# Performance work log

Measured on AMD Instinct MI355X. Metric: run time of the kernel, lower is better.

The kernel has to match this reference:

```python
import jax, jax.numpy as jnp
import numpy as np

B, C, L = 4, 64, 4096
RED = 4          # reduction -> q/k channels = C // RED = 16
N_HASHES = 4
HASH_BUCKETS = min(L // 4, 32)  # = 32, matches torch code
EPS = 1e-5


def _conv1x1(x, W, b):
    # x: [B, Cin, L], W: [Cout, Cin], b: [Cout]
    return jnp.einsum('bcl,oc->bol', x, W) + b[None, :, None]


def setup_inputs() -> dict:
    key = jax.random.key(0)
    ks = jax.random.split(key, 12)
    Cq = C // RED
    x = jax.random.normal(ks[0], (B, C, L), dtype=jnp.float32)
    hash_idx = jax.random.randint(ks[1], (B, N_HASHES, L), 0, HASH_BUCKETS, dtype=jnp.int32)
    sC = 1.0 / np.sqrt(C)
    Wq = jax.random.normal(ks[2], (Cq, C), dtype=jnp.float32) * sC
    bq = jax.random.normal(ks[3], (Cq,), dtype=jnp.float32) * 0.01
    Wk = jax.random.normal(ks[4], (Cq, C), dtype=jnp.float32) * sC
    bk = jax.random.normal(ks[5], (Cq,), dtype=jnp.float32) * 0.01
    Wv = jax.random.normal(ks[6], (C, C), dtype=jnp.float32) * sC
    bv = jax.random.normal(ks[7], (C,), dtype=jnp.float32) * 0.01
    Wo = jax.random.normal(ks[8], (C, C), dtype=jnp.float32) * sC
    bo = jax.random.normal(ks[9], (C,), dtype=jnp.float32) * 0.01
    gamma = jax.random.normal(ks[10], (1,), dtype=jnp.float32)  # nonzero so attn path matters
    bn_w = jnp.ones((C,), dtype=jnp.float32)
    bn_b = jnp.zeros((C,), dtype=jnp.float32)
    return dict(x=x, hash_idx=hash_idx, Wq=Wq, bq=bq, Wk=Wk, bk=bk,
                Wv=Wv, bv=bv, Wo=Wo, bo=bo, gamma=gamma, bn_w=bn_w, bn_b=bn_b)


def reference(x, hash_idx, Wq, bq, Wk, bk, Wv, bv, Wo, bo, gamma, bn_w, bn_b):
    # 1x1 conv projections
    q = _conv1x1(x, Wq, bq)   # [B, C/RED, L]
    k = _conv1x1(x, Wk, bk)   # [B, C/RED, L]
    v = _conv1x1(x, Wv, bv)   # [B, C, L]

    qT = q.transpose(0, 2, 1)  # [B, L, Cq]
    kT = k.transpose(0, 2, 1)
    vT = v.transpose(0, 2, 1)  # [B, L, C]

    # raw scores are hash-independent; only the bucket mask changes per hash
    scores = jnp.einsum('bic,bjc->bij', qT, kT)  # [B, L, L], no sqrt(d) scaling (matches torch)

    n_hashes = hash_idx.shape[1]
    acc = jnp.zeros_like(vT)
    for h in range(n_hashes):  # small fixed loop
        idx = hash_idx[:, h, :]                       # [B, L]
        mask = idx[:, :, None] == idx[:, None, :]     # same-bucket mask [B, L, L]
        s = jnp.where(mask, scores, -1e9)
        attn = jax.nn.softmax(s, axis=-1)             # within-bucket softmax (diag always valid)
        acc = acc + jnp.einsum('bij,bjc->bic', attn, vT)
    attn_out = (acc / n_hashes).transpose(0, 2, 1)    # [B, C, L], averaged over hashes

    out = _conv1x1(attn_out, Wo, bo)
    out = gamma * out + x                             # residual with learned scalar

    # BatchNorm1d, training mode: biased batch stats over (B, L) per channel
    mean = out.mean(axis=(0, 2), keepdims=True)
    var = out.var(axis=(0, 2), keepdims=True)
    out = (out - mean) * jax.lax.rsqrt(var + EPS)
    out = out * bn_w[None, :, None] + bn_b[None, :, None]
    return out
```

## Files before the change

kernel.cpp:

```cpp
#include <hip/hip_runtime.h>
#include <math.h>

#define Bn 4
#define Cn 64
#define Ln 4096
#define CQ 16
#define NH 4
#define NB 32
#define EPSV 1e-5f

#define MAXS 384
#define SFULL 192

#define QSZ   (Bn*Ln*CQ)
#define VSZ   (Bn*Ln*Cn)
#define ACCSZ (Bn*Ln*Cn)
#define NBH   (Bn*NH)

#define OFF_K   QSZ
#define OFF_V   (2*QSZ)
#define OFF_ACC (2*QSZ + VSZ)

#define LOG2E 1.44269504088896f

__global__ __launch_bounds__(256) void proj_kernel(
        const float* __restrict__ x,
        const float* __restrict__ Wq, const float* __restrict__ bq,
        const float* __restrict__ Wk, const float* __restrict__ bk,
        const float* __restrict__ Wv, const float* __restrict__ bv,
        float* __restrict__ q, float* __restrict__ k, float* __restrict__ v) {
    __shared__ float sWt[Cn*32];
    __shared__ float sb[32];
    int tid = threadIdx.x;
    int third = blockIdx.x % 3;
    int pg    = blockIdx.x / 3;
    int rbase = third * 32;
    for (int idx = tid; idx < Cn*32; idx += 256) {
        int rr = idx & 31, c = idx >> 5;
        int r = rbase + rr;
        float w;
        if (r < 16)      w = Wq[r*Cn + c];
        else if (r < 32) w = Wk[(r-16)*Cn + c];
        else             w = Wv[(r-32)*Cn + c];
        sWt[c*32 + rr] = w;
    }
    if (tid < 32) {
        int r = rbase + tid;
        sb[tid] = (r < 16) ? bq[r] : (r < 32 ? bk[r-16] : bv[r-32]);
    }
    __syncthreads();
    int p = tid & 63, og = tid >> 6;
    int gp = pg * 64 + p;
    int b = gp >> 12, l = gp & (Ln - 1);
    const float* xp = &x[b*Cn*Ln + l];
    int rr0 = og * 8;
    float val[8];
    #pragma unroll
    for (int i = 0; i < 8; i++) val[i] = sb[rr0 + i];
    #pragma unroll
    for (int c0 = 0; c0 < Cn; c0 += 8) {
        float xv[8];
        #pragma unroll
        for (int i = 0; i < 8; i++) xv[i] = xp[(c0 + i)*Ln];
        #pragma unroll
        for (int i = 0; i < 8; i++) {
            const float4 wa = *(const float4*)&sWt[(c0 + i)*32 + rr0];
            const float4 wb = *(const float4*)&sWt[(c0 + i)*32 + rr0 + 4];
            float xvi = xv[i];
            val[0] = fmaf(wa.x, xvi, val[0]); val[1] = fmaf(wa.y, xvi, val[1]);
            val[2] = fmaf(wa.z, xvi, val[2]); val[3] = fmaf(wa.w, xvi, val[3]);
            val[4] = fmaf(wb.x, xvi, val[4]); val[5] = fmaf(wb.y, xvi, val[5]);
            val[6] = fmaf(wb.z, xvi, val[6]); val[7] = fmaf(wb.w, xvi, val[7]);
        }
    }
    int f = third*8 + og*2;
    float4 t0 = make_float4(val[0], val[1], val[2], val[3]);
    float4 t1 = make_float4(val[4], val[5], val[6], val[7]);
    float4* q4 = (float4*)&q[gp*CQ];
    float4* k4 = (float4*)&k[gp*CQ];
    float4* v4 = (float4*)&v[gp*Cn];
    if (f < 4)      { q4[f]   = t0; q4[f+1] = t1; }
    else if (f < 8) { k4[f-4] = t0; k4[f-3] = t1; }
    else            { v4[f-8] = t0; v4[f-7] = t1; }
}

__device__ __forceinline__ float quad_reduce_sum(float d) {
    d += __int_as_float(__builtin_amdgcn_mov_dpp(__float_as_int(d), 0xB1, 0xF, 0xF, true));
    d += __int_as_float(__builtin_amdgcn_mov_dpp(__float_as_int(d), 0x4E, 0xF, 0xF, true));
    return d;
}

__device__ __forceinline__ float rowsum16(float x) {
    x += __int_as_float(__builtin_amdgcn_mov_dpp(__float_as_int(x), 0x114, 0xF, 0xF, true));
    x += __int_as_float(__builtin_amdgcn_mov_dpp(__float_as_int(x), 0x118, 0xF, 0xF, true));
    return x;
}

struct SweepState {
    float4 qr[4];
    float4 o[4][4];
    float  lsum[4];
    int    ir[4];
};

__device__ __forceinline__ void sweep_init(SweepState& st, int q0, int S, int act,
        const int* list, const float4* Q4, int qq, int c4) {
    #pragma unroll
    for (int s = 0; s < 4; s++) {
        int qi = q0 + s*4 + qq;
        int a = act && (qi < S);
        st.ir[s] = a ? list[qi] : -1;
        float4 t = make_float4(0.f, 0.f, 0.f, 0.f);
        if (a) {
            t = Q4[(size_t)st.ir[s]*4 + c4];
            t.x *= LOG2E; t.y *= LOG2E; t.z *= LOG2E; t.w *= LOG2E;
        }
        st.qr[s] = t;
        st.lsum[s] = 0.f;
        #pragma unroll
        for (int tt = 0; tt < 4; tt++) st.o[s][tt] = make_float4(0.f, 0.f, 0.f, 0.f);
    }
}

template<bool MASKED>
__device__ __forceinline__ void kb_step(SweepState& st, int kb, int nkv,
        const float4* ks4, const float4* vs4, int l15, int kk,
        int i0, int i1, int i2, int i3) {
    const float4 kq = ks4[kb*16 + l15];
    const float4 va = vs4[kb*64 + i0*16 + l15];
    const float4 vb = vs4[kb*64 + i1*16 + l15];
    const float4 vc = vs4[kb*64 + i2*16 + l15];
    const float4 vd = vs4[kb*64 + i3*16 + l15];
    #pragma unroll
    for (int s = 0; s < 4; s++) {
        float d = st.qr[s].x * kq.x;
        d = fmaf(st.qr[s].y, kq.y, d);
        d = fmaf(st.qr[s].z, kq.z, d);
        d = fmaf(st.qr[s].w, kq.w, d);
        d = quad_reduce_sum(d);
        float pw = __builtin_amdgcn_exp2f(d);
        if (MASKED) pw = ((kb*4 + kk) < nkv) ? pw : 0.f;
        st.lsum[s] += pw;
        st.o[s][0].x = fmaf(pw, va.x, st.o[s][0].x); st.o[s][0].y = fmaf(pw, va.y, st.o[s][0].y);
        st.o[s][0].z = fmaf(pw, va.z, st.o[s][0].z); st.o[s][0].w = fmaf(pw, va.w, st.o[s][0].w);
        st.o[s][1].x = fmaf(pw, vb.x, st.o[s][1].x); st.o[s][1].y = fmaf(pw, vb.y, st.o[s][1].y);
        st.o[s][1].z = fmaf(pw, vb.z, st.o[s][1].z); st.o[s][1].w = fmaf(pw, vb.w, st.o[s][1].w);
        st.o[s][2].x = fmaf(pw, vc.x, st.o[s][2].x); st.o[s][2].y = fmaf(pw, vc.y, st.o[s][2].y);
        st.o[s][2].z = fmaf(pw, vc.z, st.o[s][2].z); st.o[s][2].w = fmaf(pw, vc.w, st.o[s][2].w);
        st.o[s][3].x = fmaf(pw, vd.x, st.o[s][3].x); st.o[s][3].y = fmaf(pw, vd.y, st.o[s][3].y);
        st.o[s][3].z = fmaf(pw, vd.z, st.o[s][3].z); st.o[s][3].w = fmaf(pw, vd.w, st.o[s][3].w);
    }
}

__device__ __forceinline__ void sweep_keys(SweepState& st, int nk,
        const float4* ks4, const float4* vs4, int l15, int kk,
        int i0, int i1, int i2, int i3) {
    int nf = nk >> 2;
    for (int kb = 0; kb < nf; kb++)
        kb_step<false>(st, kb, nk, ks4, vs4, l15, kk, i0, i1, i2, i3);
    if (nk & 3)
        kb_step<true>(st, nf, nk, ks4, vs4, l15, kk, i0, i1, i2, i3);
}

template<int MODE>
__device__ __forceinline__ void sweep_fin(SweepState& st, float* __restrict__ acc,
        int b, int h, int qq, int lane, int c4) {
    #pragma unroll
    for (int s = 0; s < 4; s++) {
        st.lsum[s] = rowsum16(st.lsum[s]);
        #pragma unroll
        for (int t = 0; t < 4; t++) {
            st.o[s][t].x = rowsum16(st.o[s][t].x);
            st.o[s][t].y = rowsum16(st.o[s][t].y);
            st.o[s][t].z = rowsum16(st.o[s][t].z);
            st.o[s][t].w = rowsum16(st.o[s][t].w);
        }
    }
    if ((lane & 15) < 12) return;
    #pragma unroll
    for (int s = 0; s < 4; s++) {
        if (st.ir[s] >= 0) {
            float inv = 1.f / st.lsum[s];
            #pragma unroll
            for (int t = 0; t < 4; t++) {
                float4 r;
                r.x = st.o[s][t].x * inv; r.y = st.o[s][t].y * inv;
                r.z = st.o[s][t].z * inv; r.w = st.o[s][t].w * inv;
                int ch = ((qq + t) & 3)*16 + c4*4;
                if (MODE == 1) {
                    *(float4*)&acc[(((size_t)h*Bn + b)*Ln + st.ir[s])*Cn + ch] = r;
                } else {
                    float* ap = &acc[((size_t)b*Ln + st.ir[s])*Cn + ch];
                    atomicAdd(&ap[0], r.x); atomicAdd(&ap[1], r.y);
                    atomicAdd(&ap[2], r.z); atomicAdd(&ap[3], r.w);
                }
            }
        }
    }
}

__device__ __forceinline__ void stage_kv(int tid, int nk, int k0, const int* list,
        const float4* K4, const float4* V4, float4* ks4, float4* vs4) {
    const float4 z = make_float4(0.f, 0.f, 0.f, 0.f);
    int nb4 = (nk + 3) >> 2;
    for (int G = tid; G < nb4*16; G += 512) {
        int j = G >> 2;
        ks4[G] = (j < nk) ? K4[(size_t)list[k0 + j]*4 + (G & 3)] : z;
    }
    for (int F = tid; F < nb4*64; F += 512) {
        int kb = F >> 6, ii = (F >> 4) & 3, k2 = (F >> 2) & 3, cc = F & 3;
        int j = kb*4 + k2;
        vs4[F] = (j < nk) ? V4[(size_t)list[k0 + j]*16 + ii*4 + cc] : z;
    }
}

template<int MODE>
__global__ __launch_bounds__(512, 2) void attn_kernel(
        const float* __restrict__ q, const float* __restrict__ k,
        const float* __restrict__ v, const int* __restrict__ hidx,
        float* __restrict__ acc) {
    __shared__ int list[MAXS];
    __shared__ int wtot[8];
    __shared__ float4 ks4[SFULL*4];
    __shared__ float4 vs4[SFULL*16];
    int blk = blockIdx.x;
    int u  = blk & (NB-1);
    int bh = blk >> 5;
    int b  = bh >> 2;
    int h  = bh & 3;
    int tid = threadIdx.x;

    const int4* hp4 = (const int4*)&hidx[bh*Ln + tid*8];
    int hv[8];
    #pragma unroll
    for (int t = 0; t < 2; t++) {
        int4 tmp = hp4[t];
        hv[t*4+0]=tmp.x; hv[t*4+1]=tmp.y; hv[t*4+2]=tmp.z; hv[t*4+3]=tmp.w;
    }
    int myCnt = 0;
    #pragma unroll
    for (int t = 0; t < 8; t++) myCnt += (hv[t] == u);
    int lane = tid & 63, wv = tid >> 6;
    int pre = myCnt;
    #pragma unroll
    for (int d = 1; d < 64; d <<= 1) {
        int t = __shfl_up(pre, d, 64);
        if (lane >= d) pre += t;
    }
    if (lane == 63) wtot[wv] = pre;
    __syncthreads();
    int base = 0, Sall = 0;
    #pragma unroll
    for (int w = 0; w < 8; w++) {
        base += (w < wv) ? wtot[w] : 0;
        Sall += wtot[w];
    }
    int S = min(Sall, MAXS);
    int excl = base + pre - myCnt;
    #pragma unroll
    for (int t = 0; t < 8; t++) {
        if (hv[t] == u) {
            if (excl < MAXS) list[excl] = tid*8 + t;
            excl++;
        }
    }
    __syncthreads();

    int qq = (lane >> 4) & 3;
    int kk = (lane >> 2) & 3;
    int c4 = lane & 3;
    int l15 = lane & 15;
    int i0 = qq, i1 = (qq+1)&3, i2 = (qq+2)&3, i3 = (qq+3)&3;
    const float4* Q4 = (const float4*)&q[(size_t)b*Ln*CQ];
    const float4* K4 = (const float4*)&k[(size_t)b*Ln*CQ];
    const float4* V4 = (const float4*)&v[(size_t)b*Ln*Cn];

    if (S <= SFULL) {
        stage_kv(tid, S, 0, list, K4, V4, ks4, vs4);
        __syncthreads();
        for (int q0 = wv*16; q0 < S; q0 += 128) {
            SweepState st;
            sweep_init(st, q0, S, 1, list, Q4, qq, c4);
            sweep_keys(st, S, ks4, vs4, l15, kk, i0, i1, i2, i3);
            sweep_fin<MODE>(st, acc, b, h, qq, lane, c4);
        }
    } else {
        for (int q0s = 0; q0s < S; q0s += 128) {
            int q0 = q0s + wv*16;
            int act = q0 < S;
            SweepState st;
            sweep_init(st, q0, S, act, list, Q4, qq, c4);
            for (int k0 = 0; k0 < S; k0 += SFULL) {
                int nk = min(SFULL, S - k0);
                __syncthreads();
                stage_kv(tid, nk, k0, list, K4, V4, ks4, vs4);
                __syncthreads();
                if (act) sweep_keys(st, nk, ks4, vs4, l15, kk, i0, i1, i2, i3);
            }
            if (act) sweep_fin<MODE>(st, acc, b, h, qq, lane, c4);
        }
    }
}

template<int MODE>
__global__ __launch_bounds__(256) void outconv_kernel(
        const float* __restrict__ acc, const float* __restrict__ Wo,
        const float* __restrict__ bo, const float* __restrict__ gamma,
        const float* __restrict__ x, float* __restrict__ y) {
    __shared__ float sWt[Cn*Cn];
    __shared__ float sA[Cn*33];
    __shared__ float sb[Cn];
    int tid = threadIdx.x;
    int pg = blockIdx.x;
    for (int idx = tid; idx < Cn*Cn; idx += 256) {
        int o = idx & 63, c = idx >> 6;
        sWt[c*Cn + o] = Wo[o*Cn + c];
    }
    if (tid < Cn) sb[tid] = bo[tid];
    const float4* a4 = (const float4*)&acc[(size_t)pg*32*Cn];
    #pragma unroll
    for (int r = 0; r < 2; r++) {
        int idx = r*256 + tid;
        int p = idx >> 4, c0 = (idx & 15) * 4;
        float4 t = a4[idx];
        if (MODE == 1) {
            float4 t1 = a4[(size_t)ACCSZ/4   + idx];
            float4 t2 = a4[(size_t)ACCSZ/4*2 + idx];
            float4 t3 = a4[(size_t)ACCSZ/4*3 + idx];
            t.x += t1.x + t2.x + t3.x; t.y += t1.y + t2.y + t3.y;
            t.z += t1.z + t2.z + t3.z; t.w += t1.w + t2.w + t3.w;
        }
        sA[(c0+0)*33 + p] = t.x*0.25f;
        sA[(c0+1)*33 + p] = t.y*0.25f;
        sA[(c0+2)*33 + p] = t.z*0.25f;
        sA[(c0+3)*33 + p] = t.w*0.25f;
    }
    __syncthreads();
    float g = gamma[0];
    int p = tid & 31, og = tid >> 5;
    int gp = pg * 32 + p;
    int b = gp >> 12, l = gp & (Ln - 1);
    int o0 = og * 8;
    float val[8];
    #pragma unroll
    for (int i = 0; i < 8; i++) val[i] = sb[o0 + i];
    #pragma unroll
    for (int c = 0; c < Cn; c++) {
        float av = sA[c*33 + p];
        const float4 wa = *(const float4*)&sWt[c*Cn + o0];
        const float4 wb = *(const float4*)&sWt[c*Cn + o0 + 4];
        val[0] = fmaf(wa.x, av, val[0]); val[1] = fmaf(wa.y, av, val[1]);
        val[2] = fmaf(wa.z, av, val[2]); val[3] = fmaf(wa.w, av, val[3]);
        val[4] = fmaf(wb.x, av, val[4]); val[5] = fmaf(wb.y, av, val[5]);
        val[6] = fmaf(wb.z, av, val[6]); val[7] = fmaf(wb.w, av, val[7]);
    }
    #pragma unroll
    for (int i = 0; i < 8; i++) {
        int o = o0 + i;
        float yv = fmaf(g, val[i], x[(b*Cn + o)*Ln + l]);
        y[(b*Cn + o)*Ln + l] = yv;
    }
}

__global__ __launch_bounds__(256) void stats_kernel(
        const float* __restrict__ y, float* __restrict__ ssumP, float* __restrict__ ssqP) {
    int c = blockIdx.x >> 2;
    int part = blockIdx.x & 3;
    int tid = threadIdx.x;
    const float4* yp = (const float4*)&y[(part*Cn + c)*Ln];
    float s = 0.f, s2 = 0.f;
    #pragma unroll
    for (int i = 0; i < 4; i++) {
        float4 t = yp[i*256 + tid];
        s  += t.x + t.y + t.z + t.w;
        s2 += t.x*t.x + t.y*t.y + t.z*t.z + t.w*t.w;
    }
    #pragma unroll
    for (int w = 1; w < 64; w <<= 1) {
        s  += __shfl_xor(s,  w, 64);
        s2 += __shfl_xor(s2, w, 64);
    }
    __shared__ float rs[4], rs2[4];
    int wv = tid >> 6;
    if ((tid & 63) == 0) { rs[wv] = s; rs2[wv] = s2; }
    __syncthreads();
    if (tid == 0) {
        ssumP[blockIdx.x] = rs[0]+rs[1]+rs[2]+rs[3];
        ssqP[blockIdx.x]  = rs2[0]+rs2[1]+rs2[2]+rs2[3];
    }
}

__global__ __launch_bounds__(256) void norm_kernel(
        const float* __restrict__ y,
        const float* __restrict__ ssumP, const float* __restrict__ ssqP,
        const float* __restrict__ bnw, const float* __restrict__ bnb,
        float* __restrict__ out) {
    int idx = blockIdx.x * 256 + threadIdx.x;
    int flat = idx * 4;
    int c = (flat >> 12) & 63;
    float s = 0.f, s2 = 0.f;
    #pragma unroll
    for (int hh = 0; hh < 4; hh++) { s += ssumP[c*4+hh]; s2 += ssqP[c*4+hh]; }
    const float n = (float)(Bn*Ln);
    float mu = s / n;
    float var = s2 / n - mu*mu;
    float is = rsqrtf(var + EPSV);
    float w = is * bnw[c];
    float bb = bnb[c] - mu * w;
    float4 t = ((const float4*)y)[idx];
    float4 r;
    r.x = t.x*w + bb; r.y = t.y*w + bb; r.z = t.z*w + bb; r.w = t.w*w + bb;
    ((float4*)out)[idx] = r;
}

extern "C" void kernel_launch(void* const* d_in, const int* in_sizes, int n_in,
                              void* d_out, int out_size, void* d_ws, size_t ws_size,
                              hipStream_t stream) {
    const float* x    = (const float*)d_in[0];
    const int*   hidx = (const int*)  d_in[1];
    const float* Wq   = (const float*)d_in[2];
    const float* bq   = (const float*)d_in[3];
    const float* Wk   = (const float*)d_in[4];
    const float* bk   = (const float*)d_in[5];
    const float* Wv   = (const float*)d_in[6];
    const float* bv   = (const float*)d_in[7];
    const float* Wo   = (const float*)d_in[8];
    const float* bo   = (const float*)d_in[9];
    const float* gam  = (const float*)d_in[10];
    const float* bnw  = (const float*)d_in[11];
    const float* bnb  = (const float*)d_in[12];
    float* out = (float*)d_out;

    float* ws  = (float*)d_ws;
    float* q   = ws;
    float* k   = ws + OFF_K;
    float* v   = ws + OFF_V;
    float* acc = ws + OFF_ACC;
    float* y   = ws;

    const size_t bigNeed = ((size_t)OFF_ACC + 4*(size_t)ACCSZ + 512) * sizeof(float);
    bool big = ws_size >= bigNeed;
    float* ssumP = acc + (big ? 4*(size_t)ACCSZ : (size_t)ACCSZ);
    float* ssqP  = ssumP + 256;

    proj_kernel<<<Bn*Ln/64*3, 256, 0, stream>>>(x, Wq, bq, Wk, bk, Wv, bv, q, k, v);
    if (big) {
        attn_kernel<1><<<NBH*NB, 512, 0, stream>>>(q, k, v, hidx, acc);
        outconv_kernel<1><<<Bn*Ln/32, 256, 0, stream>>>(acc, Wo, bo, gam, x, y);
    } else {
        hipMemsetAsync(acc, 0, (size_t)ACCSZ*sizeof(float), stream);
        attn_kernel<0><<<NBH*NB, 512, 0, stream>>>(q, k, v, hidx, acc);
        outconv_kernel<0><<<Bn*Ln/32, 256, 0, stream>>>(acc, Wo, bo, gam, x, y);
    }
    stats_kernel<<<Cn*4, 256, 0, stream>>>(y, ssumP, ssqP);
    norm_kernel<<<Bn*Cn*Ln/4/256, 256, 0, stream>>>(y, ssumP, ssqP, bnw, bnb, out);
}
```

Before: 156.7 us.

## Prefetch next key block and rebalance tail queries across waves with single-row sweeps

Software-prefetches the next key/value block from shared memory into registers while computing the current one, so LDS latency can overlap the exp and FMA work. In the fits-in-LDS path, each wave handles its first 16 queries as before. Queries beyond the first 128 are then spread over all waves in groups of 4 rows instead of 16, which reduces load imbalance when bucket sizes are just above 128. The price is more registers for the prefetch buffers and more passes over the key/value tile for tail queries.

```diff
diff --git a/kernel.cpp b/kernel.cpp
--- a/kernel.cpp
+++ b/kernel.cpp
@@ -96,17 +96,18 @@
     return x;
 }
 
-struct SweepState {
-    float4 qr[4];
-    float4 o[4][4];
-    float  lsum[4];
-    int    ir[4];
+template<int NS> struct Sweep {
+    float4 qr[NS];
+    float4 o[NS][4];
+    float  lsum[NS];
+    int    ir[NS];
 };
 
-__device__ __forceinline__ void sweep_init(SweepState& st, int q0, int S, int act,
+template<int NS>
+__device__ __forceinline__ void sweep_init(Sweep<NS>& st, int q0, int S, int act,
         const int* list, const float4* Q4, int qq, int c4) {
     #pragma unroll
-    for (int s = 0; s < 4; s++) {
+    for (int s = 0; s < NS; s++) {
         int qi = q0 + s*4 + qq;
         int a = act && (qi < S);
         st.ir[s] = a ? list[qi] : -1;
@@ -122,17 +123,12 @@
     }
 }
 
-template<bool MASKED>
-__device__ __forceinline__ void kb_step(SweepState& st, int kb, int nkv,
-        const float4* ks4, const float4* vs4, int l15, int kk,
-        int i0, int i1, int i2, int i3) {
-    const float4 kq = ks4[kb*16 + l15];
-    const float4 va = vs4[kb*64 + i0*16 + l15];
-    const float4 vb = vs4[kb*64 + i1*16 + l15];
-    const float4 vc = vs4[kb*64 + i2*16 + l15];
-    const float4 vd = vs4[kb*64 + i3*16 + l15];
-    #pragma unroll
-    for (int s = 0; s < 4; s++) {
+template<int NS, bool MASKED>
+__device__ __forceinline__ void kb_compute(Sweep<NS>& st, int kb, int nkv, int kk,
+        const float4& kq, const float4& va, const float4& vb,
+        const float4& vc, const float4& vd) {
+    #pragma unroll
+    for (int s = 0; s < NS; s++) {
         float d = st.qr[s].x * kq.x;
         d = fmaf(st.qr[s].y, kq.y, d);
         d = fmaf(st.qr[s].z, kq.z, d);
@@ -152,21 +148,37 @@
     }
 }
 
-__device__ __forceinline__ void sweep_keys(SweepState& st, int nk,
+template<int NS>
+__device__ __forceinline__ void sweep_keys(Sweep<NS>& st, int nk,
         const float4* ks4, const float4* vs4, int l15, int kk,
         int i0, int i1, int i2, int i3) {
+    int nb = (nk + 3) >> 2;
     int nf = nk >> 2;
-    for (int kb = 0; kb < nf; kb++)
-        kb_step<false>(st, kb, nk, ks4, vs4, l15, kk, i0, i1, i2, i3);
+    if (nb <= 0) return;
+    float4 kq = ks4[l15];
+    float4 va = vs4[i0*16 + l15];
+    float4 vb = vs4[i1*16 + l15];
+    float4 vc = vs4[i2*16 + l15];
+    float4 vd = vs4[i3*16 + l15];
+    for (int kb = 0; kb < nf; kb++) {
+        int kb1 = min(kb + 1, nb - 1);
+        float4 kq2 = ks4[kb1*16 + l15];
+        float4 va2 = vs4[kb1*64 + i0*16 + l15];
+        float4 vb2 = vs4[kb1*64 + i1*16 + l15];
+        float4 vc2 = vs4[kb1*64 + i2*16 + l15];
+        float4 vd2 = vs4[kb1*64 + i3*16 + l15];
+        kb_compute<NS,false>(st, kb, nk, kk, kq, va, vb, vc, vd);
+        kq = kq2; va = va2; vb = vb2; vc = vc2; vd = vd2;
+    }
     if (nk & 3)
-        kb_step<true>(st, nf, nk, ks4, vs4, l15, kk, i0, i1, i2, i3);
-}
-
-template<int MODE>
-__device__ __forceinline__ void sweep_fin(SweepState& st, float* __restrict__ acc,
+        kb_compute<NS,true>(st, nf, nk, kk, kq, va, vb, vc, vd);
+}
+
+template<int NS, int MODE>
+__device__ __forceinline__ void sweep_fin(Sweep<NS>& st, float* __restrict__ acc,
         int b, int h, int qq, int lane, int c4) {
     #pragma unroll
-    for (int s = 0; s < 4; s++) {
+    for (int s = 0; s < NS; s++) {
         st.lsum[s] = rowsum16(st.lsum[s]);
         #pragma unroll
         for (int t = 0; t < 4; t++) {
@@ -178,7 +190,7 @@
     }
     if ((lane & 15) < 12) return;
     #pragma unroll
-    for (int s = 0; s < 4; s++) {
+    for (int s = 0; s < NS; s++) {
         if (st.ir[s] >= 0) {
             float inv = 1.f / st.lsum[s];
             #pragma unroll
@@ -199,6 +211,18 @@
     }
 }
 
+template<int NS, int MODE>
+__device__ __forceinline__ void run_sweep(int q0, int S, int act,
+        const int* list, const float4* Q4,
+        const float4* ks4, const float4* vs4, float* __restrict__ acc,
+        int b, int h, int qq, int lane, int c4, int l15, int kk,
+        int i0, int i1, int i2, int i3) {
+    Sweep<NS> st;
+    sweep_init<NS>(st, q0, S, act, list, Q4, qq, c4);
+    sweep_keys<NS>(st, S, ks4, vs4, l15, kk, i0, i1, i2, i3);
+    sweep_fin<NS,MODE>(st, acc, b, h, qq, lane, c4);
+}
+
 __device__ __forceinline__ void stage_kv(int tid, int nk, int k0, const int* list,
         const float4* K4, const float4* V4, float4* ks4, float4* vs4) {
     const float4 z = make_float4(0.f, 0.f, 0.f, 0.f);
@@ -278,26 +302,26 @@
     if (S <= SFULL) {
         stage_kv(tid, S, 0, list, K4, V4, ks4, vs4);
         __syncthreads();
-        for (int q0 = wv*16; q0 < S; q0 += 128) {
-            SweepState st;
-            sweep_init(st, q0, S, 1, list, Q4, qq, c4);
-            sweep_keys(st, S, ks4, vs4, l15, kk, i0, i1, i2, i3);
-            sweep_fin<MODE>(st, acc, b, h, qq, lane, c4);
-        }
+        if (wv*16 < S)
+            run_sweep<4,MODE>(wv*16, S, 1, list, Q4, ks4, vs4, acc,
+                              b, h, qq, lane, c4, l15, kk, i0, i1, i2, i3);
+        for (int qb = 128 + wv*4; qb < S; qb += 32)
+            run_sweep<1,MODE>(qb, S, 1, list, Q4, ks4, vs4, acc,
+                              b, h, qq, lane, c4, l15, kk, i0, i1, i2, i3);
     } else {
         for (int q0s = 0; q0s < S; q0s += 128) {
             int q0 = q0s + wv*16;
             int act = q0 < S;
-            SweepState st;
-            sweep_init(st, q0, S, act, list, Q4, qq, c4);
+            Sweep<4> st;
+            sweep_init<4>(st, q0, S, act, list, Q4, qq, c4);
             for (int k0 = 0; k0 < S; k0 += SFULL) {
                 int nk = min(SFULL, S - k0);
                 __syncthreads();
                 stage_kv(tid, nk, k0, list, K4, V4, ks4, vs4);
                 __syncthreads();
-                if (act) sweep_keys(st, nk, ks4, vs4, l15, kk, i0, i1, i2, i3);
+                if (act) sweep_keys<4>(st, nk, ks4, vs4, l15, kk, i0, i1, i2, i3);
             }
-            if (act) sweep_fin<MODE>(st, acc, b, h, qq, lane, c4);
+            if (act) sweep_fin<4,MODE>(st, acc, b, h, qq, lane, c4);
         }
     }
 }
```

After: 158.7 us. Within noise of the previous version (+1.3%).
